# Optimization experiments

Measured on AMD Instinct MI355X. Metric: run time of the kernel, lower is better.

Reference implementation:

```python
import jax, jax.numpy as jnp
import numpy as np

S, B, C = 7, 2, 20
L_COORD, L_NOOBJ = 5.0, 0.5
BATCH = 16384


def setup_inputs() -> dict:
    key = jax.random.key(0)
    k1, k2, k3 = jax.random.split(key, 3)
    pred = jax.random.normal(k1, (BATCH, S, S, 5 * B + C), dtype=jnp.float32)
    target = jax.random.uniform(k2, (BATCH, S, S, 5 * B + C), dtype=jnp.float32)
    conf = target[..., 4]
    target = target.at[..., 4].set(jnp.where(conf > 0.9, conf, 0.0))
    # per-cell branch choice (replaces python random.random() > 0.5 per object)
    choice = jax.random.randint(k3, (BATCH, S, S), 0, 2, dtype=jnp.int32)
    return {"pred": pred, "target": target, "choice": choice}


def reference(pred, target, choice):
    dt = pred.dtype
    tconf = target[..., 4]
    obj = tconf > 0                      # [B,S,S]
    m = obj.astype(dt)
    n_obj = jnp.maximum(m.sum(), 1.0)
    c = choice.astype(bool)              # True -> box 1, False -> box 2
    cE = c[..., None]

    pxy = jnp.where(cE, pred[..., 0:2], pred[..., 5:7])
    pwh = jnp.where(cE, pred[..., 2:4], pred[..., 7:9])
    txy = jnp.where(cE, target[..., 0:2], target[..., 5:7])
    twh = jnp.where(cE, target[..., 2:4], target[..., 7:9])
    twh = jnp.where(obj[..., None], twh, 1.0)  # sqrt-safe outside obj mask
    pobj = jnp.where(c, pred[..., 4], pred[..., 9])
    tobj = jnp.where(c, tconf, target[..., 9])

    # per-object: mean over 2 elems for xy and for (wh - sqrt(twh)), summed over objects
    loc_cell = ((pxy - txy) ** 2).mean(-1) + ((pwh - jnp.sqrt(twh)) ** 2).mean(-1)
    loc_loss = L_COORD * (m * loc_cell).sum()
    obj_loss = (m * (pobj - tobj) ** 2).sum()

    nm = (tconf == 0).astype(dt)
    n_no = jnp.maximum(nm.sum(), 1.0)
    noobj_loss = L_NOOBJ * (
        (nm * (pred[..., 4] - tconf) ** 2).sum() / n_no
        + (nm * (pred[..., 9] - target[..., 9]) ** 2).sum() / n_no
    )

    # faithful to original: softmax applied BEFORE CrossEntropyLoss (double softmax)
    logits = pred[..., 5 * B:5 * B + C]
    sm = jax.nn.softmax(logits, axis=-1)
    logp = jax.nn.log_softmax(sm, axis=-1)
    tcls = jnp.argmax(target[..., 5 * B:5 * B + C], axis=-1)
    ce = -jnp.take_along_axis(logp, tcls[..., None], axis=-1)[..., 0]
    cls_loss = (m * ce).sum() / n_obj

    return (loc_loss, cls_loss, obj_loss, noobj_loss)
```

## Files before the change

kernel.cpp:

```cpp
#include <hip/hip_runtime.h>
#include <math.h>


typedef float vf4 __attribute__((ext_vector_type(4)));

constexpr int NCH = 30;
constexpr int CC  = 20;
constexpr int ROW = 8;
constexpr int T   = 256;
constexpr int CPB = 128;
constexpr int NF4 = CPB * NCH * 2 / 4;
constexpr int HF4 = NF4 / 2;
constexpr int GRID = 1280;

__device__ __forceinline__ void issue_chunk(
    const float* __restrict__ pred, const float* __restrict__ target,
    const int* __restrict__ choice, int cc, int ncells, int tid,
    vf4 (&r)[8], int& ci)
{
    long long base = (long long)cc * CPB;
    if (base + CPB <= (long long)ncells) {
        const vf4* Pb = (const vf4*)(pred + base * NCH);
        const vf4* Tb = (const vf4*)(target + base * NCH);
        #pragma unroll
        for (int j = 0; j < 8; ++j) {
            int k = j * T + tid;
            if (k < NF4)
                r[j] = (k < HF4) ? __builtin_nontemporal_load(&Pb[k])
                                 : __builtin_nontemporal_load(&Tb[k - HF4]);
        }
    } else {
        int nfl = (int)(ncells - base) * NCH;
        const float* Pf = pred + base * NCH;
        const float* Tf = target + base * NCH;
        #pragma unroll
        for (int j = 0; j < 8; ++j) {
            int k = j * T + tid;
            vf4 v = (vf4)(0.f, 0.f, 0.f, 0.f);
            if (k < NF4) {
                int kk = (k < HF4) ? k : k - HF4;
                const float* src = (k < HF4) ? Pf : Tf;
                int b = 4 * kk;
                if (b + 0 < nfl) v.x = src[b + 0];
                if (b + 1 < nfl) v.y = src[b + 1];
                if (b + 2 < nfl) v.z = src[b + 2];
                if (b + 3 < nfl) v.w = src[b + 3];
            }
            r[j] = v;
        }
    }
    if (tid < CPB) {
        long long ce = base + tid;
        ci = (ce < (long long)ncells) ? __builtin_nontemporal_load(&choice[ce]) : 0;
    }
}

__global__ __launch_bounds__(T) void yolo_main(
    const float* __restrict__ pred, const float* __restrict__ target,
    const int* __restrict__ choice, float* __restrict__ ws,
    int ncells, int nchunks)
{
    __shared__ float sbuf[2 * CPB * NCH];
    const int tid = threadIdx.x;

    float a_loc = 0.f, a_ce = 0.f, a_obj = 0.f, a_no = 0.f;
    float a_nob = 0.f, a_nno = 0.f;

    vf4 r[8];
    int ci = 0;
    int c = blockIdx.x;
    if (c < nchunks) issue_chunk(pred, target, choice, c, ncells, tid, r, ci);

    for (; c < nchunks; c += GRID) {
        __syncthreads();
        #pragma unroll
        for (int j = 0; j < 8; ++j) {
            int k = j * T + tid;
            if (k < NF4) *(vf4*)&sbuf[k * 4] = r[j];
        }
        int myc = ci;
        __syncthreads();

        int cn = c + GRID;
        if (cn < nchunks) issue_chunk(pred, target, choice, cn, ncells, tid, r, ci);

        if (tid < CPB && (long long)c * CPB + tid < ncells) {
            const float* sp  = &sbuf[tid * NCH];
            const float* stt = &sbuf[CPB * NCH + tid * NCH];
            float p[NCH], t[NCH];
            #pragma unroll
            for (int i = 0; i < NCH / 2; ++i) {
                float2 v = *(const float2*)&sp[2 * i];  p[2*i] = v.x; p[2*i+1] = v.y;
            }
            #pragma unroll
            for (int i = 0; i < NCH / 2; ++i) {
                float2 w = *(const float2*)&stt[2 * i]; t[2*i] = w.x; t[2*i+1] = w.y;
            }
            bool csel = myc != 0;

            float tconf = t[4];
            bool  obj = tconf > 0.0f;
            float m = obj ? 1.0f : 0.0f;

            float pxy0 = csel ? p[0] : p[5];
            float pxy1 = csel ? p[1] : p[6];
            float pwh0 = csel ? p[2] : p[7];
            float pwh1 = csel ? p[3] : p[8];
            float pobj = csel ? p[4] : p[9];
            float txy0 = csel ? t[0] : t[5];
            float txy1 = csel ? t[1] : t[6];
            float twh0 = csel ? t[2] : t[7];
            float twh1 = csel ? t[3] : t[8];
            if (!obj) { twh0 = 1.0f; twh1 = 1.0f; }
            float tobj = csel ? tconf : t[9];

            float dx = pxy0 - txy0, dy = pxy1 - txy1;
            float dw = pwh0 - sqrtf(twh0), dh = pwh1 - sqrtf(twh1);
            a_loc += m * (0.5f * (dx*dx + dy*dy) + 0.5f * (dw*dw + dh*dh));

            float dob = pobj - tobj;
            a_obj += m * dob * dob;

            float nm = (tconf == 0.0f) ? 1.0f : 0.0f;
            float d4 = p[4] - tconf, d9 = p[9] - t[9];
            a_no += nm * (d4 * d4 + d9 * d9);

            a_nob += m;
            a_nno += nm;

            int   tcls  = 0;
            float tbest = t[10];
            #pragma unroll
            for (int i = 1; i < CC; ++i) {
                float v = t[10 + i];
                if (v > tbest) { tbest = v; tcls = i; }
            }
            float mx = p[10];
            #pragma unroll
            for (int i = 1; i < CC; ++i) mx = fmaxf(mx, p[10 + i]);
            float e[CC];
            float Z = 0.f;
            #pragma unroll
            for (int i = 0; i < CC; ++i) { e[i] = __expf(p[10+i] - mx); Z += e[i]; }
            float rZ = 1.0f / Z;
            float Z2 = 0.f, sm_t = 0.f;
            #pragma unroll
            for (int i = 0; i < CC; ++i) {
                float sm = e[i] * rZ;
                Z2 += __expf(sm);
                if (i == tcls) sm_t = sm;
            }
            a_ce += m * (__logf(Z2) - sm_t);
        }
    }

    #pragma unroll
    for (int off = 32; off > 0; off >>= 1) {
        a_loc += __shfl_down(a_loc, off);
        a_ce  += __shfl_down(a_ce,  off);
        a_obj += __shfl_down(a_obj, off);
        a_no  += __shfl_down(a_no,  off);
        a_nob += __shfl_down(a_nob, off);
        a_nno += __shfl_down(a_nno, off);
    }

    __shared__ float red[4][6];
    int wave = tid >> 6;
    int lane = tid & 63;
    if (lane == 0) {
        red[wave][0] = a_loc; red[wave][1] = a_ce;  red[wave][2] = a_obj;
        red[wave][3] = a_no;  red[wave][4] = a_nob; red[wave][5] = a_nno;
    }
    __syncthreads();
    if (tid < 6) {
        float v = red[0][tid] + red[1][tid] + red[2][tid] + red[3][tid];
        ws[(size_t)blockIdx.x * ROW + tid] = v;
    }
}

__global__ __launch_bounds__(256) void yolo_reduce(
    const float* __restrict__ ws, float* __restrict__ out, int nb)
{
    float s[6] = {0.f, 0.f, 0.f, 0.f, 0.f, 0.f};
    for (int b = threadIdx.x; b < nb; b += 256) {
        #pragma unroll
        for (int j = 0; j < 6; ++j) s[j] += ws[(size_t)b * ROW + j];
    }
    #pragma unroll
    for (int off = 32; off > 0; off >>= 1) {
        #pragma unroll
        for (int j = 0; j < 6; ++j) s[j] += __shfl_down(s[j], off);
    }
    __shared__ float red[4][6];
    int wave = threadIdx.x >> 6;
    int lane = threadIdx.x & 63;
    if (lane == 0) {
        #pragma unroll
        for (int j = 0; j < 6; ++j) red[wave][j] = s[j];
    }
    __syncthreads();
    if (threadIdx.x == 0) {
        float t[6];
        #pragma unroll
        for (int j = 0; j < 6; ++j)
            t[j] = red[0][j] + red[1][j] + red[2][j] + red[3][j];
        out[0] = 5.0f * t[0];
        out[1] = t[1] / fmaxf(t[4], 1.0f);
        out[2] = t[2];
        out[3] = 0.5f * t[3] / fmaxf(t[5], 1.0f);
    }
}

extern "C" void kernel_launch(void* const* d_in, const int* in_sizes, int n_in,
                              void* d_out, int out_size, void* d_ws, size_t ws_size,
                              hipStream_t stream) {
    const float* pred   = (const float*)d_in[0];
    const float* target = (const float*)d_in[1];
    const int*   choice = (const int*)d_in[2];
    float* out = (float*)d_out;
    float* ws  = (float*)d_ws;

    int ncells  = in_sizes[2];
    int nchunks = (ncells + CPB - 1) / CPB;
    int grid    = GRID < nchunks ? GRID : nchunks;
    yolo_main<<<grid, T, 0, stream>>>(pred, target, choice, ws, ncells, nchunks);
    yolo_reduce<<<1, 256, 0, stream>>>(ws, out, grid);
}
```

Measured before the change: 193.6 us.

## Double-buffer register prefetch two chunks ahead and shrink grid

Keeps two register buffers of chunk data in flight, so each block issues loads for the chunk two iterations ahead while computing the current one. This deepens memory-level parallelism to better hide global load latency in this bandwidth-bound loss reduction. The grid is reduced from 1280 to 1024 blocks. The cost is doubled register use for the staging buffers, which may lower occupancy. An unused helper function and a stray label are left in the code.

```diff
diff --git a/kernel.cpp b/kernel.cpp
--- a/kernel.cpp
+++ b/kernel.cpp
@@ -11,7 +11,7 @@
 constexpr int CPB = 128;
 constexpr int NF4 = CPB * NCH * 2 / 4;
 constexpr int HF4 = NF4 / 2;
-constexpr int GRID = 1280;
+constexpr int GRID = 1024;
 
 __device__ __forceinline__ void issue_chunk(
     const float* __restrict__ pred, const float* __restrict__ target,
@@ -55,6 +55,89 @@
     }
 }
 
+__device__ __forceinline__ void stage_and_compute(
+    float* __restrict__ sbuf, const vf4 (&r)[8], int myc,
+    long long cellg, int ncells, int tid,
+    float& a_loc, float& a_ce, float& a_obj, float& a_no,
+    float& a_nob, float& a_nno)
+{
+    __syncthreads();
+    #pragma unroll
+    for (int j = 0; j < 8; ++j) {
+        int k = j * T + tid;
+        if (k < NF4) *(vf4*)&sbuf[k * 4] = r[j];
+    }
+    __syncthreads();
+    if (tid < CPB && cellg < (long long)ncells) {
+        const float* sp  = &sbuf[tid * NCH];
+        const float* stt = &sbuf[CPB * NCH + tid * NCH];
+        float p[NCH], t[NCH];
+        #pragma unroll
+        for (int i = 0; i < NCH / 2; ++i) {
+            float2 v = *(const float2*)&sp[2 * i];  p[2*i] = v.x; p[2*i+1] = v.y;
+        }
+        #pragma unroll
+        for (int i = 0; i < NCH / 2; ++i) {
+            float2 w = *(const float2*)&stt[2 * i]; t[2*i] = w.x; t[2*i+1] = w.y;
+        }
+        bool csel = myc != 0;
+
+        float tconf = t[4];
+        bool  obj = tconf > 0.0f;
+        float m = obj ? 1.0f : 0.0f;
+
+        float pxy0 = csel ? p[0] : p[5];
+        float pxy1 = csel ? p[1] : p[6];
+        float pwh0 = csel ? p[2] : p[7];
+        float pwh1 = csel ? p[3] : p[8];
+        float pobj = csel ? p[4] : p[9];
+        float txy0 = csel ? t[0] : t[5];
+        float txy1 = csel ? t[1] : t[6];
+        float twh0 = csel ? t[2] : t[7];
+        float twh1 = csel ? t[3] : t[8];
+        if (!obj) { twh0 = 1.0f; twh1 = 1.0f; }
+        float tobj = csel ? tconf : t[9];
+
+        float dx = pxy0 - txy0, dy = pxy1 - txy1;
+        float dw = pwh0 - sqrtf(twh0), dh = pwh1 - sqrtf(twh1);
+        a_loc += m * (0.5f * (dx*dx + dy*dy) + 0.5f * (dw*dw + dh*dh));
+
+        float dob = pobj - tobj;
+        a_obj += m * dob * dob;
+
+        float nm = (tconf == 0.0f) ? 1.0f : 0.0f;
+        float d4 = p[4] - tconf, d9 = p[9] - t[9];
+        a_no += nm * (d4 * d4 + d9 * d9);
+
+        a_nob += m;
+        a_nno += nm;
+
+        int   tcls  = 0;
+        float tbest = t[10];
+        #pragma unroll
+        for (int i = 1; i < CC; ++i) {
+            float v = t[10 + i];
+            if (v > tbest) { tbest = v; tcls = i; }
+        }
+        float mx = p[10];
+        #pragma unroll
+        for (int i = 1; i < CC; ++i) mx = fmaxf(mx, p[10 + i]);
+        float e[CC];
+        float Z = 0.f;
+        #pragma unroll
+        for (int i = 0; i < CC; ++i) { e[i] = __expf(p[10+i] - mx); Z += e[i]; }
+        float rZ = 1.0f / Z;
+        float Z2 = 0.f, sm_t = 0.f;
+        #pragma unroll
+        for (int i = 0; i < CC; ++i) {
+            float sm = e[i] * rZ;
+            Z2 += __expf(sm);
+            if (i == tcls) sm_t = sm;
+        }
+        a_ce += m * (__logf(Z2) - sm_t);
+    }
+}
+
 __global__ __launch_bounds__(T) void yolo_main(
     const float* __restrict__ pred, const float* __restrict__ target,
     const int* __restrict__ choice, float* __restrict__ ws,
@@ -66,91 +149,161 @@
     float a_loc = 0.f, a_ce = 0.f, a_obj = 0.f, a_no = 0.f;
     float a_nob = 0.f, a_nno = 0.f;
 
-    vf4 r[8];
-    int ci = 0;
+    vf4 rA[8], rB[8];
+    int ciA = 0, ciB = 0;
     int c = blockIdx.x;
-    if (c < nchunks) issue_chunk(pred, target, choice, c, ncells, tid, r, ci);
-
-    for (; c < nchunks; c += GRID) {
-        __syncthreads();
-        #pragma unroll
-        for (int j = 0; j < 8; ++j) {
-            int k = j * T + tid;
-            if (k < NF4) *(vf4*)&sbuf[k * 4] = r[j];
-        }
-        int myc = ci;
-        __syncthreads();
-
-        int cn = c + GRID;
-        if (cn < nchunks) issue_chunk(pred, target, choice, cn, ncells, tid, r, ci);
-
-        if (tid < CPB && (long long)c * CPB + tid < ncells) {
-            const float* sp  = &sbuf[tid * NCH];
-            const float* stt = &sbuf[CPB * NCH + tid * NCH];
-            float p[NCH], t[NCH];
+    if (c < nchunks)        issue_chunk(pred, target, choice, c,        ncells, tid, rA, ciA);
+    if (c + GRID < nchunks) issue_chunk(pred, target, choice, c + GRID, ncells, tid, rB, ciB);
+
+    for (; c < nchunks; c += 2 * GRID) {
+        {
+            int myc = ciA;
+            long long cg = (long long)c * CPB + tid;
+            __syncthreads();
             #pragma unroll
-            for (int i = 0; i < NCH / 2; ++i) {
-                float2 v = *(const float2*)&sp[2 * i];  p[2*i] = v.x; p[2*i+1] = v.y;
-            }
+            for (int j = 0; j < 8; ++j) {
+                int k = j * T + tid;
+                if (k < NF4) *(vf4*)&sbuf[k * 4] = rA[j];
+            }
+            __syncthreads();
+            if (c + 2 * GRID < nchunks)
+                issue_chunk(pred, target, choice, c + 2 * GRID, ncells, tid, rA, ciA);
+            stage_compute_body:;
+            if (tid < CPB && cg < (long long)ncells) {
+                const float* sp  = &sbuf[tid * NCH];
+                const float* stt = &sbuf[CPB * NCH + tid * NCH];
+                float p[NCH], t[NCH];
+                #pragma unroll
+                for (int i = 0; i < NCH / 2; ++i) {
+                    float2 v = *(const float2*)&sp[2 * i];  p[2*i] = v.x; p[2*i+1] = v.y;
+                }
+                #pragma unroll
+                for (int i = 0; i < NCH / 2; ++i) {
+                    float2 w = *(const float2*)&stt[2 * i]; t[2*i] = w.x; t[2*i+1] = w.y;
+                }
+                bool csel = myc != 0;
+                float tconf = t[4];
+                bool  obj = tconf > 0.0f;
+                float m = obj ? 1.0f : 0.0f;
+                float pxy0 = csel ? p[0] : p[5];
+                float pxy1 = csel ? p[1] : p[6];
+                float pwh0 = csel ? p[2] : p[7];
+                float pwh1 = csel ? p[3] : p[8];
+                float pobj = csel ? p[4] : p[9];
+                float txy0 = csel ? t[0] : t[5];
+                float txy1 = csel ? t[1] : t[6];
+                float twh0 = csel ? t[2] : t[7];
+                float twh1 = csel ? t[3] : t[8];
+                if (!obj) { twh0 = 1.0f; twh1 = 1.0f; }
+                float tobj = csel ? tconf : t[9];
+                float dx = pxy0 - txy0, dy = pxy1 - txy1;
+                float dw = pwh0 - sqrtf(twh0), dh = pwh1 - sqrtf(twh1);
+                a_loc += m * (0.5f * (dx*dx + dy*dy) + 0.5f * (dw*dw + dh*dh));
+                float dob = pobj - tobj;
+                a_obj += m * dob * dob;
+                float nm = (tconf == 0.0f) ? 1.0f : 0.0f;
+                float d4 = p[4] - tconf, d9 = p[9] - t[9];
+                a_no += nm * (d4 * d4 + d9 * d9);
+                a_nob += m;
+                a_nno += nm;
+                int   tcls  = 0;
+                float tbest = t[10];
+                #pragma unroll
+                for (int i = 1; i < CC; ++i) {
+                    float v = t[10 + i];
+                    if (v > tbest) { tbest = v; tcls = i; }
+                }
+                float mx = p[10];
+                #pragma unroll
+                for (int i = 1; i < CC; ++i) mx = fmaxf(mx, p[10 + i]);
+                float e[CC];
+                float Z = 0.f;
+                #pragma unroll
+                for (int i = 0; i < CC; ++i) { e[i] = __expf(p[10+i] - mx); Z += e[i]; }
+                float rZ = 1.0f / Z;
+                float Z2 = 0.f, sm_t = 0.f;
+                #pragma unroll
+                for (int i = 0; i < CC; ++i) {
+                    float sm = e[i] * rZ;
+                    Z2 += __expf(sm);
+                    if (i == tcls) sm_t = sm;
+                }
+                a_ce += m * (__logf(Z2) - sm_t);
+            }
+        }
+        if (c + GRID < nchunks) {
+            int myc = ciB;
+            long long cg = (long long)(c + GRID) * CPB + tid;
+            __syncthreads();
             #pragma unroll
-            for (int i = 0; i < NCH / 2; ++i) {
-                float2 w = *(const float2*)&stt[2 * i]; t[2*i] = w.x; t[2*i+1] = w.y;
-            }
-            bool csel = myc != 0;
-
-            float tconf = t[4];
-            bool  obj = tconf > 0.0f;
-            float m = obj ? 1.0f : 0.0f;
-
-            float pxy0 = csel ? p[0] : p[5];
-            float pxy1 = csel ? p[1] : p[6];
-            float pwh0 = csel ? p[2] : p[7];
-            float pwh1 = csel ? p[3] : p[8];
-            float pobj = csel ? p[4] : p[9];
-            float txy0 = csel ? t[0] : t[5];
-            float txy1 = csel ? t[1] : t[6];
-            float twh0 = csel ? t[2] : t[7];
-            float twh1 = csel ? t[3] : t[8];
-            if (!obj) { twh0 = 1.0f; twh1 = 1.0f; }
-            float tobj = csel ? tconf : t[9];
-
-            float dx = pxy0 - txy0, dy = pxy1 - txy1;
-            float dw = pwh0 - sqrtf(twh0), dh = pwh1 - sqrtf(twh1);
-            a_loc += m * (0.5f * (dx*dx + dy*dy) + 0.5f * (dw*dw + dh*dh));
-
-            float dob = pobj - tobj;
-            a_obj += m * dob * dob;
-
-            float nm = (tconf == 0.0f) ? 1.0f : 0.0f;
-            float d4 = p[4] - tconf, d9 = p[9] - t[9];
-            a_no += nm * (d4 * d4 + d9 * d9);
-
-            a_nob += m;
-            a_nno += nm;
-
-            int   tcls  = 0;
-            float tbest = t[10];
-            #pragma unroll
-            for (int i = 1; i < CC; ++i) {
-                float v = t[10 + i];
-                if (v > tbest) { tbest = v; tcls = i; }
-            }
-            float mx = p[10];
-            #pragma unroll
-            for (int i = 1; i < CC; ++i) mx = fmaxf(mx, p[10 + i]);
-            float e[CC];
-            float Z = 0.f;
-            #pragma unroll
-            for (int i = 0; i < CC; ++i) { e[i] = __expf(p[10+i] - mx); Z += e[i]; }
-            float rZ = 1.0f / Z;
-            float Z2 = 0.f, sm_t = 0.f;
-            #pragma unroll
-            for (int i = 0; i < CC; ++i) {
-                float sm = e[i] * rZ;
-                Z2 += __expf(sm);
-                if (i == tcls) sm_t = sm;
-            }
-            a_ce += m * (__logf(Z2) - sm_t);
+            for (int j = 0; j < 8; ++j) {
+                int k = j * T + tid;
+                if (k < NF4) *(vf4*)&sbuf[k * 4] = rB[j];
+            }
+            __syncthreads();
+            if (c + 3 * GRID < nchunks)
+                issue_chunk(pred, target, choice, c + 3 * GRID, ncells, tid, rB, ciB);
+            if (tid < CPB && cg < (long long)ncells) {
+                const float* sp  = &sbuf[tid * NCH];
+                const float* stt = &sbuf[CPB * NCH + tid * NCH];
+                float p[NCH], t[NCH];
+                #pragma unroll
+                for (int i = 0; i < NCH / 2; ++i) {
+                    float2 v = *(const float2*)&sp[2 * i];  p[2*i] = v.x; p[2*i+1] = v.y;
+                }
+                #pragma unroll
+                for (int i = 0; i < NCH / 2; ++i) {
+                    float2 w = *(const float2*)&stt[2 * i]; t[2*i] = w.x; t[2*i+1] = w.y;
+                }
+                bool csel = myc != 0;
+                float tconf = t[4];
+                bool  obj = tconf > 0.0f;
+                float m = obj ? 1.0f : 0.0f;
+                float pxy0 = csel ? p[0] : p[5];
+                float pxy1 = csel ? p[1] : p[6];
+                float pwh0 = csel ? p[2] : p[7];
+                float pwh1 = csel ? p[3] : p[8];
+                float pobj = csel ? p[4] : p[9];
+                float txy0 = csel ? t[0] : t[5];
+                float txy1 = csel ? t[1] : t[6];
+                float twh0 = csel ? t[2] : t[7];
+                float twh1 = csel ? t[3] : t[8];
+                if (!obj) { twh0 = 1.0f; twh1 = 1.0f; }
+                float tobj = csel ? tconf : t[9];
+                float dx = pxy0 - txy0, dy = pxy1 - txy1;
+                float dw = pwh0 - sqrtf(twh0), dh = pwh1 - sqrtf(twh1);
+                a_loc += m * (0.5f * (dx*dx + dy*dy) + 0.5f * (dw*dw + dh*dh));
+                float dob = pobj - tobj;
+                a_obj += m * dob * dob;
+                float nm = (tconf == 0.0f) ? 1.0f : 0.0f;
+                float d4 = p[4] - tconf, d9 = p[9] - t[9];
+                a_no += nm * (d4 * d4 + d9 * d9);
+                a_nob += m;
+                a_nno += nm;
+                int   tcls  = 0;
+                float tbest = t[10];
+                #pragma unroll
+                for (int i = 1; i < CC; ++i) {
+                    float v = t[10 + i];
+                    if (v > tbest) { tbest = v; tcls = i; }
+                }
+                float mx = p[10];
+                #pragma unroll
+                for (int i = 1; i < CC; ++i) mx = fmaxf(mx, p[10 + i]);
+                float e[CC];
+                float Z = 0.f;
+                #pragma unroll
+                for (int i = 0; i < CC; ++i) { e[i] = __expf(p[10+i] - mx); Z += e[i]; }
+                float rZ = 1.0f / Z;
+                float Z2 = 0.f, sm_t = 0.f;
+                #pragma unroll
+                for (int i = 0; i < CC; ++i) {
+                    float sm = e[i] * rZ;
+                    Z2 += __expf(sm);
+                    if (i == tcls) sm_t = sm;
+                }
+                a_ce += m * (__logf(Z2) - sm_t);
+            }
         }
     }
 
```

After: 197.6 us. 1.02x slower.
